# Kernel optimization log

Hardware: AMD Instinct MI355X
Metric: run time of the kernel (lower is better)

## Reference

```python
import jax, jax.numpy as jnp
import numpy as np

B, S, H, E, K = 4, 2048, 1024, 8, 2


def setup_inputs() -> dict:
    key = jax.random.key(0)
    k_hs, k_eo, k_w1, k_w2 = jax.random.split(key, 4)
    return {
        "hidden_states": jax.random.normal(k_hs, (B, S, H), dtype=jnp.float32),
        "expert_outputs": jax.random.normal(k_eo, (E, B, S, H), dtype=jnp.float32),
        "W1": jax.random.normal(k_w1, (H, H), dtype=jnp.float32) * 0.02,
        "b1": jnp.zeros((H,), dtype=jnp.float32),
        "W2": jax.random.normal(k_w2, (H, E), dtype=jnp.float32) * 0.02,
        "b2": jnp.zeros((E,), dtype=jnp.float32),
        "k": K,
    }


def reference(hidden_states, expert_outputs, W1, b1, W2, b2, k):
    # Router MLP (eval mode: dropout is identity, no noise)
    h = jax.nn.relu(hidden_states @ W1 + b1)          # [B,S,H]
    router_logits = h @ W2 + b2                        # [B,S,E]
    router_probs = jax.nn.softmax(router_logits, axis=-1)
    top_k_gates, top_k_indices = jax.lax.top_k(router_probs, k)  # [B,S,k]
    n_experts = expert_outputs.shape[0]
    # Scatter top-k gates into a dense [B,S,E] gate matrix (same math as the
    # per-expert masked accumulation in the torch loop)
    onehot = jax.nn.one_hot(top_k_indices, n_experts, dtype=top_k_gates.dtype)  # [B,S,k,E]
    gate_mat = jnp.einsum('bsk,bske->bse', top_k_gates, onehot)
    combined = jnp.einsum('bse,ebsd->bsd', gate_mat, expert_outputs)
    return combined
```

## Files before the change

### kernel.cpp

```cpp
#include <hip/hip_runtime.h>
#include <math.h>


#define H_DIM 1024
#define E_NUM 8

typedef __attribute__((ext_vector_type(8))) short s16x8;
typedef __attribute__((ext_vector_type(8))) unsigned short u16x8;
typedef __attribute__((ext_vector_type(4))) float f32x4;

__device__ __forceinline__ unsigned short f2bf(float x) {
    unsigned int u = __float_as_uint(x);
    unsigned int r = (u + 0x7FFFu + ((u >> 16) & 1u)) >> 16;
    return (unsigned short)r;
}
__device__ __forceinline__ float bf2f(unsigned short b) {
    return __uint_as_float(((unsigned int)b) << 16);
}

__device__ __forceinline__ void gload_lds16(const void* g, void* lds) {
    __builtin_amdgcn_global_load_lds(
        (const __attribute__((address_space(1))) void*)g,
        (__attribute__((address_space(3))) void*)lds, 16, 0, 0);
}

__global__ __launch_bounds__(256) void prep_a_kernel(
    const float* __restrict__ A, char* __restrict__ img)
{
    int t = blockIdx.x * 256 + threadIdx.x;
    int m = t >> 7;
    int k = (t & 127) << 3;
    const float* src = A + ((size_t)m << 10) + k;
    float4 v0 = *reinterpret_cast<const float4*>(src);
    float4 v1 = *reinterpret_cast<const float4*>(src + 4);
    float xs[8] = {v0.x, v0.y, v0.z, v0.w, v1.x, v1.y, v1.z, v1.w};
    u16x8 hv, lv;
    #pragma unroll
    for (int j = 0; j < 8; ++j) {
        unsigned short h = f2bf(xs[j]);
        hv[j] = h;
        lv[j] = f2bf(xs[j] - bf2f(h));
    }
    int rb = m >> 7, mr = m & 127, kt = k >> 5, s = (k >> 3) & 3;
    char* base = img + (((size_t)(rb * 32 + kt)) << 14) + mr * 128;
    *reinterpret_cast<u16x8*>(base + ((s ^ (mr & 7)) << 4)) = hv;
    *reinterpret_cast<u16x8*>(base + (((s + 4) ^ (mr & 7)) << 4)) = lv;
}

__global__ __launch_bounds__(256) void prep_b_kernel(
    const float* __restrict__ W, char* __restrict__ img)
{
    int t = blockIdx.x * 256 + threadIdx.x;
    int n = t & 1023;
    int k = (t >> 10) << 3;
    u16x8 hv, lv;
    #pragma unroll
    for (int j = 0; j < 8; ++j) {
        float x = W[((size_t)(k + j) << 10) + n];
        unsigned short h = f2bf(x);
        hv[j] = h;
        lv[j] = f2bf(x - bf2f(h));
    }
    int cb = n >> 7, nr = n & 127, kt = k >> 5, s = (k >> 3) & 3;
    char* base = img + (((size_t)(cb * 32 + kt)) << 14) + nr * 128;
    *reinterpret_cast<u16x8*>(base + ((s ^ (nr & 7)) << 4)) = hv;
    *reinterpret_cast<u16x8*>(base + (((s + 4) ^ (nr & 7)) << 4)) = lv;
}

__global__ __launch_bounds__(256, 2) void gemm1_mfma_kernel(
    const char* __restrict__ Aimg, const char* __restrict__ Bimg,
    const float* __restrict__ bias, float* __restrict__ Hout)
{
    __shared__ char As[16384];
    __shared__ char Bs[16384];

    int bid = blockIdx.x;
    int swz = (bid & 7) * 64 + (bid >> 3);
    int rb = swz >> 3;
    int cb = swz & 7;

    int tid = threadIdx.x;
    int lane = tid & 63;
    int wave = tid >> 6;
    int wm = (wave >> 1) * 64;
    int wn = (wave & 1) * 64;
    int l15 = lane & 15, l4 = lane >> 4;

    int aoff_h[4], aoff_l[4], boff_h[4], boff_l[4];
    #pragma unroll
    for (int f = 0; f < 4; ++f) {
        int ar = wm + f * 16 + l15;
        aoff_h[f] = ar * 128 + ((l4 ^ (ar & 7)) << 4);
        aoff_l[f] = ar * 128 + (((l4 + 4) ^ (ar & 7)) << 4);
        int br = wn + f * 16 + l15;
        boff_h[f] = br * 128 + ((l4 ^ (br & 7)) << 4);
        boff_l[f] = br * 128 + (((l4 + 4) ^ (br & 7)) << 4);
    }

    const char* abase = Aimg + (size_t)rb * (32 * 16384);
    const char* bbase = Bimg + (size_t)cb * (32 * 16384);

    f32x4 acc[4][4];
    #pragma unroll
    for (int i = 0; i < 4; ++i)
        #pragma unroll
        for (int j = 0; j < 4; ++j)
            acc[i][j] = (f32x4){0.f, 0.f, 0.f, 0.f};

    for (int kt = 0; kt < 32; ++kt) {
        const char* ga = abase + (kt << 14);
        const char* gb = bbase + (kt << 14);
        int toff = tid << 4;
        #pragma unroll
        for (int r = 0; r < 4; ++r) {
            gload_lds16(ga + (r << 12) + toff, As + (r << 12) + toff);
            gload_lds16(gb + (r << 12) + toff, Bs + (r << 12) + toff);
        }
        __syncthreads();

        s16x8 ah[4], al[4], bh[4], bl[4];
        #pragma unroll
        for (int f = 0; f < 4; ++f) {
            ah[f] = *reinterpret_cast<const s16x8*>(As + aoff_h[f]);
            al[f] = *reinterpret_cast<const s16x8*>(As + aoff_l[f]);
            bh[f] = *reinterpret_cast<const s16x8*>(Bs + boff_h[f]);
            bl[f] = *reinterpret_cast<const s16x8*>(Bs + boff_l[f]);
        }
        #pragma unroll
        for (int m = 0; m < 4; ++m)
            #pragma unroll
            for (int n = 0; n < 4; ++n) {
                acc[m][n] = __builtin_amdgcn_mfma_f32_16x16x32_bf16(ah[m], bh[n], acc[m][n], 0, 0, 0);
                acc[m][n] = __builtin_amdgcn_mfma_f32_16x16x32_bf16(ah[m], bl[n], acc[m][n], 0, 0, 0);
                acc[m][n] = __builtin_amdgcn_mfma_f32_16x16x32_bf16(al[m], bh[n], acc[m][n], 0, 0, 0);
            }
        __syncthreads();
    }

    int row0 = rb * 128 + wm;
    int col0 = cb * 128 + wn;
    float bcol[4];
    #pragma unroll
    for (int fn = 0; fn < 4; ++fn) bcol[fn] = bias[col0 + fn * 16 + l15];
    #pragma unroll
    for (int fm = 0; fm < 4; ++fm)
        #pragma unroll
        for (int r = 0; r < 4; ++r) {
            int row = row0 + fm * 16 + l4 * 4 + r;
            float* orow = Hout + ((size_t)row << 10);
            #pragma unroll
            for (int fn = 0; fn < 4; ++fn) {
                int col = col0 + fn * 16 + l15;
                orow[col] = fmaxf(acc[fm][fn][r] + bcol[fn], 0.f);
            }
        }
}

#define BM 128
#define BN 128
#define BK 16
#define PAD_LD 132

__global__ __launch_bounds__(256) void gemm1_relu_kernel(
    const float* __restrict__ A, const float* __restrict__ W,
    const float* __restrict__ bias, float* __restrict__ Hout,
    int M, int N, int K)
{
    __shared__ float As[BK][PAD_LD];
    __shared__ float Bs[BK][PAD_LD];
    const int tid = threadIdx.x;
    const int tx = tid & 15;
    const int ty = tid >> 4;
    const int row0 = blockIdx.y * BM;
    const int col0 = blockIdx.x * BN;
    float acc[8][8];
    #pragma unroll
    for (int i = 0; i < 8; ++i)
        #pragma unroll
        for (int j = 0; j < 8; ++j) acc[i][j] = 0.f;
    const int a_row = tid >> 2;
    const int a_k4  = (tid & 3) * 4;
    const int b_col4 = (tid & 31) * 4;
    const int b_kk   = tid >> 5;
    for (int k0 = 0; k0 < K; k0 += BK) {
        #pragma unroll
        for (int half = 0; half < 2; ++half) {
            int r = a_row + half * 64;
            float4 av = *reinterpret_cast<const float4*>(&A[(size_t)(row0 + r) * K + k0 + a_k4]);
            As[a_k4 + 0][r] = av.x; As[a_k4 + 1][r] = av.y;
            As[a_k4 + 2][r] = av.z; As[a_k4 + 3][r] = av.w;
        }
        #pragma unroll
        for (int half = 0; half < 2; ++half) {
            int kk = b_kk + half * 8;
            float4 bv = *reinterpret_cast<const float4*>(&W[(size_t)(k0 + kk) * N + col0 + b_col4]);
            *reinterpret_cast<float4*>(&Bs[kk][b_col4]) = bv;
        }
        __syncthreads();
        #pragma unroll
        for (int k = 0; k < BK; ++k) {
            float4 a0 = *reinterpret_cast<const float4*>(&As[k][ty * 8]);
            float4 a1 = *reinterpret_cast<const float4*>(&As[k][ty * 8 + 4]);
            float4 b0 = *reinterpret_cast<const float4*>(&Bs[k][tx * 8]);
            float4 b1 = *reinterpret_cast<const float4*>(&Bs[k][tx * 8 + 4]);
            float a[8] = {a0.x, a0.y, a0.z, a0.w, a1.x, a1.y, a1.z, a1.w};
            float b[8] = {b0.x, b0.y, b0.z, b0.w, b1.x, b1.y, b1.z, b1.w};
            #pragma unroll
            for (int i = 0; i < 8; ++i)
                #pragma unroll
                for (int j = 0; j < 8; ++j)
                    acc[i][j] = fmaf(a[i], b[j], acc[i][j]);
        }
        __syncthreads();
    }
    #pragma unroll
    for (int i = 0; i < 8; ++i) {
        int row = row0 + ty * 8 + i;
        #pragma unroll
        for (int j4 = 0; j4 < 2; ++j4) {
            int col = col0 + tx * 8 + j4 * 4;
            float4 v;
            v.x = fmaxf(acc[i][j4 * 4 + 0] + bias[col + 0], 0.f);
            v.y = fmaxf(acc[i][j4 * 4 + 1] + bias[col + 1], 0.f);
            v.z = fmaxf(acc[i][j4 * 4 + 2] + bias[col + 2], 0.f);
            v.w = fmaxf(acc[i][j4 * 4 + 3] + bias[col + 3], 0.f);
            *reinterpret_cast<float4*>(&Hout[(size_t)row * N + col]) = v;
        }
    }
}

__global__ __launch_bounds__(256) void route_combine_kernel(
    const float* __restrict__ Hbuf, const float* __restrict__ W2,
    const float* __restrict__ b2, const float* __restrict__ EO,
    float* __restrict__ Out, int M)
{
    const int t = blockIdx.x;
    const int tid = threadIdx.x;
    const int lane = tid & 63;
    const int wave = tid >> 6;
    const float* hrow = Hbuf + (size_t)t * H_DIM;

    float part[E_NUM];
    #pragma unroll
    for (int e = 0; e < E_NUM; ++e) part[e] = 0.f;
    #pragma unroll
    for (int it = 0; it < H_DIM / 256; ++it) {
        int j = tid + it * 256;
        float hv = hrow[j];
        const float* w = W2 + (size_t)j * E_NUM;
        #pragma unroll
        for (int e = 0; e < E_NUM; ++e) part[e] = fmaf(hv, w[e], part[e]);
    }
    #pragma unroll
    for (int off = 32; off > 0; off >>= 1)
        #pragma unroll
        for (int e = 0; e < E_NUM; ++e)
            part[e] += __shfl_down(part[e], off, 64);

    __shared__ float sred[4][E_NUM];
    __shared__ float s_g[2];
    __shared__ int   s_e[2];
    if (lane == 0)
        #pragma unroll
        for (int e = 0; e < E_NUM; ++e) sred[wave][e] = part[e];
    __syncthreads();

    if (tid == 0) {
        float logits[E_NUM];
        #pragma unroll
        for (int e = 0; e < E_NUM; ++e)
            logits[e] = sred[0][e] + sred[1][e] + sred[2][e] + sred[3][e] + b2[e];
        float m = logits[0];
        #pragma unroll
        for (int e = 1; e < E_NUM; ++e) m = fmaxf(m, logits[e]);
        float p[E_NUM], ssum = 0.f;
        #pragma unroll
        for (int e = 0; e < E_NUM; ++e) { p[e] = expf(logits[e] - m); ssum += p[e]; }
        float inv = 1.f / ssum;
        #pragma unroll
        for (int e = 0; e < E_NUM; ++e) p[e] *= inv;
        int e0 = 0;
        #pragma unroll
        for (int e = 1; e < E_NUM; ++e) if (p[e] > p[e0]) e0 = e;
        int e1 = (e0 == 0) ? 1 : 0;
        #pragma unroll
        for (int e = 0; e < E_NUM; ++e)
            if (e != e0 && e != e1 && p[e] > p[e1]) e1 = e;
        s_g[0] = p[e0]; s_g[1] = p[e1];
        s_e[0] = e0;    s_e[1] = e1;
    }
    __syncthreads();

    const float g0 = s_g[0], g1 = s_g[1];
    const size_t base0 = ((size_t)s_e[0] * M + t) * H_DIM;
    const size_t base1 = ((size_t)s_e[1] * M + t) * H_DIM;
    const int d = tid * 4;
    float4 x0 = *reinterpret_cast<const float4*>(&EO[base0 + d]);
    float4 x1 = *reinterpret_cast<const float4*>(&EO[base1 + d]);
    float4 o;
    o.x = g0 * x0.x + g1 * x1.x;
    o.y = g0 * x0.y + g1 * x1.y;
    o.z = g0 * x0.z + g1 * x1.z;
    o.w = g0 * x0.w + g1 * x1.w;
    *reinterpret_cast<float4*>(&Out[(size_t)t * H_DIM + d]) = o;
}

extern "C" void kernel_launch(void* const* d_in, const int* in_sizes, int n_in,
                              void* d_out, int out_size, void* d_ws, size_t ws_size,
                              hipStream_t stream)
{
    const float* hs = (const float*)d_in[0];
    const float* EO = (const float*)d_in[1];
    const float* W1 = (const float*)d_in[2];
    const float* b1 = (const float*)d_in[3];
    const float* W2 = (const float*)d_in[4];
    const float* b2 = (const float*)d_in[5];

    const int M = in_sizes[0] / H_DIM;
    float* out = (float*)d_out;

    const size_t A_IMG = (size_t)64 * 32 * 16384;
    const size_t B_IMG = (size_t)8 * 32 * 16384;
    if (M == 8192 && ws_size >= A_IMG + B_IMG) {
        char* Aimg = (char*)d_ws;
        char* Bimg = (char*)d_ws + A_IMG;
        prep_a_kernel<<<4096, 256, 0, stream>>>(hs, Aimg);
        prep_b_kernel<<<512, 256, 0, stream>>>(W1, Bimg);
        gemm1_mfma_kernel<<<512, 256, 0, stream>>>(Aimg, Bimg, b1, out);
    } else {
        dim3 grid1(H_DIM / BN, M / BM);
        gemm1_relu_kernel<<<grid1, 256, 0, stream>>>(hs, W1, b1, out, M, H_DIM, H_DIM);
    }
    route_combine_kernel<<<M, 256, 0, stream>>>(out, W2, b2, EO, out, M);
}
```

Baseline: 88.10 us.

## Fuse A/B prep kernels, reorder MFMA chains, raise GEMM occupancy hint

```diff
diff --git a/kernel.cpp b/kernel.cpp
--- a/kernel.cpp
+++ b/kernel.cpp
@@ -17,57 +17,57 @@
 __device__ __forceinline__ float bf2f(unsigned short b) {
     return __uint_as_float(((unsigned int)b) << 16);
 }
-
 __device__ __forceinline__ void gload_lds16(const void* g, void* lds) {
     __builtin_amdgcn_global_load_lds(
         (const __attribute__((address_space(1))) void*)g,
         (__attribute__((address_space(3))) void*)lds, 16, 0, 0);
 }
 
-__global__ __launch_bounds__(256) void prep_a_kernel(
-    const float* __restrict__ A, char* __restrict__ img)
-{
-    int t = blockIdx.x * 256 + threadIdx.x;
-    int m = t >> 7;
-    int k = (t & 127) << 3;
-    const float* src = A + ((size_t)m << 10) + k;
-    float4 v0 = *reinterpret_cast<const float4*>(src);
-    float4 v1 = *reinterpret_cast<const float4*>(src + 4);
-    float xs[8] = {v0.x, v0.y, v0.z, v0.w, v1.x, v1.y, v1.z, v1.w};
-    u16x8 hv, lv;
-    #pragma unroll
-    for (int j = 0; j < 8; ++j) {
-        unsigned short h = f2bf(xs[j]);
-        hv[j] = h;
-        lv[j] = f2bf(xs[j] - bf2f(h));
-    }
-    int rb = m >> 7, mr = m & 127, kt = k >> 5, s = (k >> 3) & 3;
-    char* base = img + (((size_t)(rb * 32 + kt)) << 14) + mr * 128;
-    *reinterpret_cast<u16x8*>(base + ((s ^ (mr & 7)) << 4)) = hv;
-    *reinterpret_cast<u16x8*>(base + (((s + 4) ^ (mr & 7)) << 4)) = lv;
-}
-
-__global__ __launch_bounds__(256) void prep_b_kernel(
-    const float* __restrict__ W, char* __restrict__ img)
-{
-    int t = blockIdx.x * 256 + threadIdx.x;
-    int n = t & 1023;
-    int k = (t >> 10) << 3;
-    u16x8 hv, lv;
-    #pragma unroll
-    for (int j = 0; j < 8; ++j) {
-        float x = W[((size_t)(k + j) << 10) + n];
-        unsigned short h = f2bf(x);
-        hv[j] = h;
-        lv[j] = f2bf(x - bf2f(h));
-    }
-    int cb = n >> 7, nr = n & 127, kt = k >> 5, s = (k >> 3) & 3;
-    char* base = img + (((size_t)(cb * 32 + kt)) << 14) + nr * 128;
-    *reinterpret_cast<u16x8*>(base + ((s ^ (nr & 7)) << 4)) = hv;
-    *reinterpret_cast<u16x8*>(base + (((s + 4) ^ (nr & 7)) << 4)) = lv;
-}
-
-__global__ __launch_bounds__(256, 2) void gemm1_mfma_kernel(
+__global__ __launch_bounds__(256) void prep_fused_kernel(
+    const float* __restrict__ A, const float* __restrict__ W,
+    char* __restrict__ Aimg, char* __restrict__ Bimg)
+{
+    if (blockIdx.x < 4096) {
+        int t = blockIdx.x * 256 + threadIdx.x;
+        int m = t >> 7;
+        int k = (t & 127) << 3;
+        const float* src = A + ((size_t)m << 10) + k;
+        float4 v0 = *reinterpret_cast<const float4*>(src);
+        float4 v1 = *reinterpret_cast<const float4*>(src + 4);
+        float xs[8] = {v0.x, v0.y, v0.z, v0.w, v1.x, v1.y, v1.z, v1.w};
+        u16x8 hv, lv;
+        #pragma unroll
+        for (int j = 0; j < 8; ++j) {
+            unsigned short h = f2bf(xs[j]);
+            hv[j] = h;
+            lv[j] = f2bf(xs[j] - bf2f(h));
+        }
+        int rb = m >> 7, mr = m & 127, kt = k >> 5, s = (k >> 3) & 3;
+        char* base = Aimg + (((size_t)(rb * 32 + kt)) << 14) + mr * 128;
+        *reinterpret_cast<u16x8*>(base + ((s ^ (mr & 7)) << 4)) = hv;
+        *reinterpret_cast<u16x8*>(base + (((s + 4) ^ (mr & 7)) << 4)) = lv;
+    } else {
+        int t = (blockIdx.x - 4096) * 256 + threadIdx.x;
+        int n = t & 1023;
+        int k = (t >> 10) << 3;
+        u16x8 hv, lv;
+        #pragma unroll
+        for (int j = 0; j < 8; ++j) {
+            float x = W[((size_t)(k + j) << 10) + n];
+            unsigned short h = f2bf(x);
+            hv[j] = h;
+            lv[j] = f2bf(x - bf2f(h));
+        }
+        int cb = n >> 7, nr = n & 127, kt = k >> 5, s = (k >> 3) & 3;
+        char* base = Bimg + (((size_t)(cb * 32 + kt)) << 14) + nr * 128;
+        *reinterpret_cast<u16x8*>(base + ((s ^ (nr & 7)) << 4)) = hv;
+        *reinterpret_cast<u16x8*>(base + (((s + 4) ^ (nr & 7)) << 4)) = lv;
+    }
+}
+
+#define MFMA_B16 __builtin_amdgcn_mfma_f32_16x16x32_bf16
+
+__global__ __launch_bounds__(256, 3) void gemm1_mfma_kernel(
     const char* __restrict__ Aimg, const char* __restrict__ Bimg,
     const float* __restrict__ bias, float* __restrict__ Hout)
 {
@@ -129,11 +129,18 @@
         #pragma unroll
         for (int m = 0; m < 4; ++m)
             #pragma unroll
-            for (int n = 0; n < 4; ++n) {
-                acc[m][n] = __builtin_amdgcn_mfma_f32_16x16x32_bf16(ah[m], bh[n], acc[m][n], 0, 0, 0);
-                acc[m][n] = __builtin_amdgcn_mfma_f32_16x16x32_bf16(ah[m], bl[n], acc[m][n], 0, 0, 0);
-                acc[m][n] = __builtin_amdgcn_mfma_f32_16x16x32_bf16(al[m], bh[n], acc[m][n], 0, 0, 0);
-            }
+            for (int n = 0; n < 4; ++n)
+                acc[m][n] = MFMA_B16(ah[m], bh[n], acc[m][n], 0, 0, 0);
+        #pragma unroll
+        for (int m = 0; m < 4; ++m)
+            #pragma unroll
+            for (int n = 0; n < 4; ++n)
+                acc[m][n] = MFMA_B16(ah[m], bl[n], acc[m][n], 0, 0, 0);
+        #pragma unroll
+        for (int m = 0; m < 4; ++m)
+            #pragma unroll
+            for (int n = 0; n < 4; ++n)
+                acc[m][n] = MFMA_B16(al[m], bh[n], acc[m][n], 0, 0, 0);
         __syncthreads();
     }
 
@@ -324,8 +331,7 @@
     if (M == 8192 && ws_size >= A_IMG + B_IMG) {
         char* Aimg = (char*)d_ws;
         char* Bimg = (char*)d_ws + A_IMG;
-        prep_a_kernel<<<4096, 256, 0, stream>>>(hs, Aimg);
-        prep_b_kernel<<<512, 256, 0, stream>>>(W1, Bimg);
+        prep_fused_kernel<<<4096 + 512, 256, 0, stream>>>(hs, W1, Aimg, Bimg);
         gemm1_mfma_kernel<<<512, 256, 0, stream>>>(Aimg, Bimg, b1, out);
     } else {
         dim3 grid1(H_DIM / BN, M / BM);
```

After: 86.56 us. Within noise of the previous version (-1.8%).
